# Kernel optimization log

Hardware: AMD Instinct MI355X
Metric: run time of the kernel (lower is better)

Reference implementation:

```python
import jax, jax.numpy as jnp
import numpy as np

TAU = 0.4
EPS = 1e-8


def setup_inputs() -> dict:
    key = jax.random.key(0)
    k1, k2 = jax.random.split(key)
    B, N, C, M = 4, 4096, 256, 2048
    l_feat = jax.random.normal(k1, (B, N, C), dtype=jnp.float32)
    g_feat = jax.random.normal(k2, (B, C, M), dtype=jnp.float32)
    return {"l_feat": l_feat, "g_feat": g_feat}


def reference(l_feat, g_feat):
    # l_feat: [B, N, C], g_feat: [B, C, M]
    # cosine similarity over channel dim C (torch CosineSimilarity, dim=2)
    l_norm = jnp.linalg.norm(l_feat, axis=2)          # [B, N]
    g_norm = jnp.linalg.norm(g_feat, axis=1)          # [B, M]
    dot = jnp.einsum('bnc,bcm->bnm', l_feat, g_feat)  # [B, N, M]
    cos_sim = dot / jnp.maximum(l_norm[:, :, None] * g_norm[:, None, :], EPS)
    sim = jnp.exp(cos_sim / TAU)                      # [B, N, M]
    # diag_embed(rowsum) followed by linalg.inv and bmm is exactly
    # row-wise division by the degree (row sum)
    sim = sim / jnp.sum(sim, axis=2, keepdims=True)
    # bmm(sim, g_feat^T): [B,N,M] x [B,M,C] -> [B,N,C]
    g_enh = jnp.einsum('bnm,bcm->bnc', sim, g_feat)
    return l_feat + g_enh
```

## Files before the change

kernel.cpp:

```cpp
#include <hip/hip_runtime.h>

#define B_ 4
#define N_ 4096
#define C_ 256
#define M_ 2048

typedef __attribute__((ext_vector_type(8))) short short8;
typedef __attribute__((ext_vector_type(4))) float f32x4;

union U16x8 { uint4 u4; unsigned short us[8]; short8 s8; };

__device__ __forceinline__ float bf2f(unsigned short h) {
    unsigned int u = ((unsigned int)h) << 16;
    return __builtin_bit_cast(float, u);
}
__device__ __forceinline__ unsigned short f2bf(float f) {
    unsigned int u = __builtin_bit_cast(unsigned int, f);
    u += 0x7FFFu + ((u >> 16) & 1u);
    return (unsigned short)(u >> 16);
}

#define GLB_AS(p) ((const __attribute__((address_space(1))) unsigned int*)(p))
#define LDS_AS(p) ((__attribute__((address_space(3))) unsigned int*)(p))

__global__ __launch_bounds__(256) void k_norm(const float* __restrict__ g,
                                              float* __restrict__ invgn) {
    __shared__ float red[4][64];
    const int b = blockIdx.y, m0 = blockIdx.x * 64;
    const int tid = threadIdx.x;
    const int ml = tid & 63, cq = tid >> 6;
    const float* gb = g + (size_t)b * C_ * M_ + m0 + ml;
    float ss = 0.f;
#pragma unroll 8
    for (int i = 0; i < 64; ++i) {
        float v = gb[(size_t)(cq * 64 + i) * M_];
        ss += v * v;
    }
    red[cq][ml] = ss;
    __syncthreads();
    if (cq == 0) {
        float t = red[0][ml] + red[1][ml] + red[2][ml] + red[3][ml];
        invgn[b * M_ + m0 + ml] = 1.f / fmaxf(sqrtf(t), 1e-8f);
    }
}

__global__ __launch_bounds__(256) void k_cast(const float* __restrict__ g,
                                              const float* __restrict__ invgn,
                                              unsigned short* __restrict__ gcm,
                                              unsigned short* __restrict__ gmc) {
    __shared__ unsigned short T[64 * 66];
    __shared__ float sInv[64];
    const int b = blockIdx.z, c0 = blockIdx.y * 64, m0 = blockIdx.x * 64;
    const int tid = threadIdx.x;
    if (tid < 64) sInv[tid] = invgn[b * M_ + m0 + tid];
    __syncthreads();
    const float* gbase = g + ((size_t)b * C_ + c0) * M_ + m0;
    unsigned short* gcmb = gcm + ((size_t)b * C_ + c0) * M_ + m0;
#pragma unroll
    for (int j = 0; j < 4; ++j) {
        int id = tid + 256 * j;
        int ci = id >> 4, mq = (id & 15) * 4;
        float4 v = *(const float4*)(gbase + (size_t)ci * M_ + mq);
        uint2 pk;
        pk.x = (unsigned)f2bf(v.x) | ((unsigned)f2bf(v.y) << 16);
        pk.y = (unsigned)f2bf(v.z) | ((unsigned)f2bf(v.w) << 16);
        *(uint2*)(gcmb + (size_t)ci * M_ + mq) = pk;
        T[ci * 66 + mq + 0] = f2bf(v.x * sInv[mq + 0]);
        T[ci * 66 + mq + 1] = f2bf(v.y * sInv[mq + 1]);
        T[ci * 66 + mq + 2] = f2bf(v.z * sInv[mq + 2]);
        T[ci * 66 + mq + 3] = f2bf(v.w * sInv[mq + 3]);
    }
    __syncthreads();
    unsigned short* gmcb = gmc + ((size_t)b * M_ + m0) * C_ + c0;
#pragma unroll
    for (int j = 0; j < 2; ++j) {
        int id = tid + 256 * j;
        int mr = id >> 3, cc8 = (id & 7) * 8;
        U16x8 t;
#pragma unroll
        for (int k = 0; k < 8; ++k) t.us[k] = T[(cc8 + k) * 66 + mr];
        *(uint4*)(gmcb + (size_t)mr * C_ + cc8) = t.u4;
    }
}

__global__ __launch_bounds__(256, 2) void k_main(
    const float* __restrict__ l,
    const unsigned short* __restrict__ gcm,
    const unsigned short* __restrict__ gmc,
    float* __restrict__ out)
{
    __shared__ __align__(16) unsigned short sGmc[64 * 256];
    __shared__ __align__(16) unsigned short sGcm[256 * 64];
    __shared__ __align__(16) unsigned short sP[32 * 72];
    __shared__ float sDen[2][32];

    const int tid = threadIdx.x;
    const int w = tid >> 6;
    const int lane = tid & 63;
    const int l15 = lane & 15;
    const int quad = lane >> 4;
    const int b = blockIdx.y;
    const int row0 = blockIdx.x * 32;
    const int rh = (w & 1) * 16;
    const int kh = w >> 1;

    int goffA[8], goffB[8];
#pragma unroll
    for (int i = 0; i < 8; ++i) {
        int p = (w * 8 + i) * 64 + lane;
        int rA = p >> 5;
        goffA[i] = rA * 256 + (((p & 31) ^ (rA & 31)) << 3);
        int rB = p >> 3;
        goffB[i] = rB * 2048 + (((p & 7) ^ (rB & 7)) << 3);
    }

    const unsigned short* gmc_b = gmc + (size_t)b * M_ * C_;
    const unsigned short* gcm_b = gcm + (size_t)b * C_ * M_;

    auto dmaA = [&](int m0) {
#pragma unroll
        for (int i = 0; i < 8; ++i)
            __builtin_amdgcn_global_load_lds(GLB_AS(gmc_b + (size_t)m0 * 256 + goffA[i]),
                                             LDS_AS(&sGmc[(w * 8 + i) * 512]), 16, 0, 0);
    };
    auto dmaB = [&](int m0) {
#pragma unroll
        for (int i = 0; i < 8; ++i)
            __builtin_amdgcn_global_load_lds(GLB_AS(gcm_b + (size_t)m0 + goffB[i]),
                                             LDS_AS(&sGcm[(w * 8 + i) * 512]), 16, 0, 0);
    };

    dmaA(0);
    dmaB(0);

    const float* lrow = l + ((size_t)b * N_ + row0 + rh + l15) * C_;
    U16x8 qt[8];
    float ss = 0.f;
#pragma unroll
    for (int kk = 0; kk < 8; ++kk) {
        float4 x0 = *(const float4*)(lrow + kk * 32 + quad * 8);
        float4 x1 = *(const float4*)(lrow + kk * 32 + quad * 8 + 4);
        ss += x0.x*x0.x + x0.y*x0.y + x0.z*x0.z + x0.w*x0.w;
        ss += x1.x*x1.x + x1.y*x1.y + x1.z*x1.z + x1.w*x1.w;
        qt[kk].us[0] = f2bf(x0.x); qt[kk].us[1] = f2bf(x0.y);
        qt[kk].us[2] = f2bf(x0.z); qt[kk].us[3] = f2bf(x0.w);
        qt[kk].us[4] = f2bf(x1.x); qt[kk].us[5] = f2bf(x1.y);
        qt[kk].us[6] = f2bf(x1.z); qt[kk].us[7] = f2bf(x1.w);
    }
    ss += __shfl_xor(ss, 16);
    ss += __shfl_xor(ss, 32);
    const float invl = 1.0f / fmaxf(sqrtf(ss), 1e-8f);
    short8 qf[8];
#pragma unroll
    for (int kk = 0; kk < 8; ++kk) {
        U16x8 t;
#pragma unroll
        for (int j = 0; j < 8; ++j) t.us[j] = f2bf(bf2f(qt[kk].us[j]) * invl);
        qf[kk] = t.s8;
    }

    __syncthreads();

    f32x4 zero = {0.f, 0.f, 0.f, 0.f};
    f32x4 o[2][4];
#pragma unroll
    for (int i = 0; i < 2; ++i)
#pragma unroll
        for (int j = 0; j < 4; ++j) o[i][j] = zero;
    float dl[4] = {0.f, 0.f, 0.f, 0.f};

    for (int mt = 0; mt < 32; ++mt) {
        f32x4 sa[2];
        sa[0] = zero; sa[1] = zero;
#pragma unroll
        for (int kk = 0; kk < 8; ++kk) {
#pragma unroll
            for (int ct = 0; ct < 2; ++ct) {
                const int row = kh * 32 + ct * 16 + l15;
                const int j = ((kk * 4 + quad) ^ (row & 31)) << 3;
                short8 bb = *(const short8*)&sGmc[row * 256 + j];
                sa[ct] = __builtin_amdgcn_mfma_f32_16x16x32_bf16(qf[kk], bb, sa[ct], 0, 0, 0);
            }
        }
#pragma unroll
        for (int ct = 0; ct < 2; ++ct)
#pragma unroll
            for (int r = 0; r < 4; ++r) {
                float p = exp2f(sa[ct][r] * 3.6067376022224085f);
                dl[r] += p;
                sP[(rh + quad * 4 + r) * 72 + kh * 32 + ct * 16 + l15] = f2bf(p);
            }
        __syncthreads();
        if (mt < 31) dmaA((mt + 1) * 64);

#pragma unroll
        for (int k2 = 0; k2 < 2; ++k2) {
            const int off = k2 * 32 + quad * 8;
            short8 a[2];
#pragma unroll
            for (int rt = 0; rt < 2; ++rt)
                a[rt] = *(const short8*)&sP[(rt * 16 + l15) * 72 + off];
#pragma unroll
            for (int ct = 0; ct < 4; ++ct) {
                const int crow = w * 64 + ct * 16 + l15;
                const int j = ((k2 * 4 + quad) ^ (crow & 7)) << 3;
                short8 bb = *(const short8*)&sGcm[crow * 64 + j];
#pragma unroll
                for (int rt = 0; rt < 2; ++rt)
                    o[rt][ct] = __builtin_amdgcn_mfma_f32_16x16x32_bf16(a[rt], bb, o[rt][ct], 0, 0, 0);
            }
        }
        __syncthreads();
        if (mt < 31) dmaB((mt + 1) * 64);
    }

#pragma unroll
    for (int r = 0; r < 4; ++r) {
        float d = dl[r];
        d += __shfl_xor(d, 1);
        d += __shfl_xor(d, 2);
        d += __shfl_xor(d, 4);
        d += __shfl_xor(d, 8);
        if (l15 == 0) sDen[kh][rh + quad * 4 + r] = d;
    }
    __syncthreads();

    const float* lb = l + ((size_t)b * N_ + row0) * C_;
    float* ob = out + ((size_t)b * N_ + row0) * C_;
#pragma unroll
    for (int rt = 0; rt < 2; ++rt) {
#pragma unroll
        for (int r = 0; r < 4; ++r) {
            const int row = rt * 16 + quad * 4 + r;
            const float inv = 1.f / (sDen[0][row] + sDen[1][row]);
            const size_t rbase = (size_t)row * C_;
#pragma unroll
            for (int ct = 0; ct < 4; ++ct) {
                const int c = w * 64 + ct * 16 + l15;
                ob[rbase + c] = lb[rbase + c] + o[rt][ct][r] * inv;
            }
        }
    }
}

extern "C" void kernel_launch(void* const* d_in, const int* in_sizes, int n_in,
                              void* d_out, int out_size, void* d_ws, size_t ws_size,
                              hipStream_t stream) {
    (void)in_sizes; (void)n_in; (void)out_size; (void)ws_size;
    const float* l = (const float*)d_in[0];
    const float* g = (const float*)d_in[1];
    float* outp = (float*)d_out;

    char* ws = (char*)d_ws;
    unsigned short* gmc = (unsigned short*)ws;
    unsigned short* gcm = (unsigned short*)(ws + (size_t)B_ * M_ * C_ * 2);
    float* invgn = (float*)(ws + 2 * (size_t)B_ * M_ * C_ * 2);

    k_norm<<<dim3(M_ / 64, B_), 256, 0, stream>>>(g, invgn);
    k_cast<<<dim3(M_ / 64, C_ / 64, B_), 256, 0, stream>>>(g, invgn, gcm, gmc);
    k_main<<<dim3(N_ / 32, B_), 256, 0, stream>>>(l, gcm, gmc, outp);
}
```

Before: 142.4 us.

## Repartition waves and use 32x32x16 MFMA for the second GEMM

Each wave now holds query fragments for all 32 rows and computes 16 key columns, so each LDS B-fragment read for the first GEMM feeds two MFMAs. The second GEMM switches from 16x16x32 to 32x32x16 bf16 MFMA with f32x16 accumulators, which cuts the number of LDS fragment loads and MFMA instructions per tile. The P buffer row stride changes to 68 and is read with split 8-byte loads, and the row-sum denominators are now reduced across four waves. The cost is more registers for the query fragments and the larger accumulators, which may hurt occupancy at the 2-block launch bound.

```diff
diff --git a/kernel.cpp b/kernel.cpp
--- a/kernel.cpp
+++ b/kernel.cpp
@@ -6,9 +6,11 @@
 #define M_ 2048
 
 typedef __attribute__((ext_vector_type(8))) short short8;
+typedef __attribute__((ext_vector_type(4))) short s16x4;
 typedef __attribute__((ext_vector_type(4))) float f32x4;
-
-union U16x8 { uint4 u4; unsigned short us[8]; short8 s8; };
+typedef __attribute__((ext_vector_type(16))) float f32x16;
+
+union U16x8 { uint4 u4; unsigned short us[8]; short8 s8; s16x4 s4[2]; };
 
 __device__ __forceinline__ float bf2f(unsigned short h) {
     unsigned int u = ((unsigned int)h) << 16;
@@ -18,6 +20,11 @@
     unsigned int u = __builtin_bit_cast(unsigned int, f);
     u += 0x7FFFu + ((u >> 16) & 1u);
     return (unsigned short)(u >> 16);
+}
+__device__ __forceinline__ short8 lds8(const unsigned short* p) {
+    s16x4 lo = *(const s16x4*)p;
+    s16x4 hi = *(const s16x4*)(p + 4);
+    return __builtin_shufflevector(lo, hi, 0, 1, 2, 3, 4, 5, 6, 7);
 }
 
 #define GLB_AS(p) ((const __attribute__((address_space(1))) unsigned int*)(p))
@@ -91,18 +98,18 @@
 {
     __shared__ __align__(16) unsigned short sGmc[64 * 256];
     __shared__ __align__(16) unsigned short sGcm[256 * 64];
-    __shared__ __align__(16) unsigned short sP[32 * 72];
-    __shared__ float sDen[2][32];
+    __shared__ __align__(16) unsigned short sP[32 * 68];
+    __shared__ float sDen[4][32];
 
     const int tid = threadIdx.x;
     const int w = tid >> 6;
     const int lane = tid & 63;
     const int l15 = lane & 15;
     const int quad = lane >> 4;
+    const int l31 = lane & 31;
+    const int h = lane >> 5;
     const int b = blockIdx.y;
     const int row0 = blockIdx.x * 32;
-    const int rh = (w & 1) * 16;
-    const int kh = w >> 1;
 
     int goffA[8], goffB[8];
 #pragma unroll
@@ -133,81 +140,75 @@
     dmaA(0);
     dmaB(0);
 
-    const float* lrow = l + ((size_t)b * N_ + row0 + rh + l15) * C_;
-    U16x8 qt[8];
-    float ss = 0.f;
-#pragma unroll
-    for (int kk = 0; kk < 8; ++kk) {
-        float4 x0 = *(const float4*)(lrow + kk * 32 + quad * 8);
-        float4 x1 = *(const float4*)(lrow + kk * 32 + quad * 8 + 4);
-        ss += x0.x*x0.x + x0.y*x0.y + x0.z*x0.z + x0.w*x0.w;
-        ss += x1.x*x1.x + x1.y*x1.y + x1.z*x1.z + x1.w*x1.w;
-        qt[kk].us[0] = f2bf(x0.x); qt[kk].us[1] = f2bf(x0.y);
-        qt[kk].us[2] = f2bf(x0.z); qt[kk].us[3] = f2bf(x0.w);
-        qt[kk].us[4] = f2bf(x1.x); qt[kk].us[5] = f2bf(x1.y);
-        qt[kk].us[6] = f2bf(x1.z); qt[kk].us[7] = f2bf(x1.w);
-    }
-    ss += __shfl_xor(ss, 16);
-    ss += __shfl_xor(ss, 32);
-    const float invl = 1.0f / fmaxf(sqrtf(ss), 1e-8f);
-    short8 qf[8];
-#pragma unroll
-    for (int kk = 0; kk < 8; ++kk) {
-        U16x8 t;
-#pragma unroll
-        for (int j = 0; j < 8; ++j) t.us[j] = f2bf(bf2f(qt[kk].us[j]) * invl);
-        qf[kk] = t.s8;
+    short8 qf[2][8];
+#pragma unroll
+    for (int rt = 0; rt < 2; ++rt) {
+        const float* lrow = l + ((size_t)b * N_ + row0 + rt * 16 + l15) * C_;
+        U16x8 qt[8];
+        float ss = 0.f;
+#pragma unroll
+        for (int kk = 0; kk < 8; ++kk) {
+            float4 x0 = *(const float4*)(lrow + kk * 32 + quad * 8);
+            float4 x1 = *(const float4*)(lrow + kk * 32 + quad * 8 + 4);
+            ss += x0.x*x0.x + x0.y*x0.y + x0.z*x0.z + x0.w*x0.w;
+            ss += x1.x*x1.x + x1.y*x1.y + x1.z*x1.z + x1.w*x1.w;
+            qt[kk].us[0] = f2bf(x0.x); qt[kk].us[1] = f2bf(x0.y);
+            qt[kk].us[2] = f2bf(x0.z); qt[kk].us[3] = f2bf(x0.w);
+            qt[kk].us[4] = f2bf(x1.x); qt[kk].us[5] = f2bf(x1.y);
+            qt[kk].us[6] = f2bf(x1.z); qt[kk].us[7] = f2bf(x1.w);
+        }
+        ss += __shfl_xor(ss, 16);
+        ss += __shfl_xor(ss, 32);
+        const float invl = 1.0f / fmaxf(sqrtf(ss), 1e-8f);
+#pragma unroll
+        for (int kk = 0; kk < 8; ++kk) {
+            U16x8 t;
+#pragma unroll
+            for (int j = 0; j < 8; ++j) t.us[j] = f2bf(bf2f(qt[kk].us[j]) * invl);
+            qf[rt][kk] = t.s8;
+        }
     }
 
     __syncthreads();
 
     f32x4 zero = {0.f, 0.f, 0.f, 0.f};
-    f32x4 o[2][4];
-#pragma unroll
-    for (int i = 0; i < 2; ++i)
-#pragma unroll
-        for (int j = 0; j < 4; ++j) o[i][j] = zero;
-    float dl[4] = {0.f, 0.f, 0.f, 0.f};
+    f32x16 o[2];
+#pragma unroll
+    for (int i = 0; i < 16; ++i) { o[0][i] = 0.f; o[1][i] = 0.f; }
+    float dl[2][4] = {{0.f,0.f,0.f,0.f},{0.f,0.f,0.f,0.f}};
 
     for (int mt = 0; mt < 32; ++mt) {
         f32x4 sa[2];
         sa[0] = zero; sa[1] = zero;
+        const int g1row = w * 16 + l15;
 #pragma unroll
         for (int kk = 0; kk < 8; ++kk) {
-#pragma unroll
-            for (int ct = 0; ct < 2; ++ct) {
-                const int row = kh * 32 + ct * 16 + l15;
-                const int j = ((kk * 4 + quad) ^ (row & 31)) << 3;
-                short8 bb = *(const short8*)&sGmc[row * 256 + j];
-                sa[ct] = __builtin_amdgcn_mfma_f32_16x16x32_bf16(qf[kk], bb, sa[ct], 0, 0, 0);
-            }
-        }
-#pragma unroll
-        for (int ct = 0; ct < 2; ++ct)
+            const int j = ((kk * 4 + quad) ^ (g1row & 31)) << 3;
+            short8 bb = *(const short8*)&sGmc[g1row * 256 + j];
+            sa[0] = __builtin_amdgcn_mfma_f32_16x16x32_bf16(qf[0][kk], bb, sa[0], 0, 0, 0);
+            sa[1] = __builtin_amdgcn_mfma_f32_16x16x32_bf16(qf[1][kk], bb, sa[1], 0, 0, 0);
+        }
+#pragma unroll
+        for (int rt = 0; rt < 2; ++rt)
 #pragma unroll
             for (int r = 0; r < 4; ++r) {
-                float p = exp2f(sa[ct][r] * 3.6067376022224085f);
-                dl[r] += p;
-                sP[(rh + quad * 4 + r) * 72 + kh * 32 + ct * 16 + l15] = f2bf(p);
+                float p = exp2f(sa[rt][r] * 3.6067376022224085f);
+                dl[rt][r] += p;
+                sP[(rt * 16 + quad * 4 + r) * 68 + w * 16 + l15] = f2bf(p);
             }
         __syncthreads();
+
         if (mt < 31) dmaA((mt + 1) * 64);
 
 #pragma unroll
-        for (int k2 = 0; k2 < 2; ++k2) {
-            const int off = k2 * 32 + quad * 8;
-            short8 a[2];
-#pragma unroll
-            for (int rt = 0; rt < 2; ++rt)
-                a[rt] = *(const short8*)&sP[(rt * 16 + l15) * 72 + off];
-#pragma unroll
-            for (int ct = 0; ct < 4; ++ct) {
-                const int crow = w * 64 + ct * 16 + l15;
-                const int j = ((k2 * 4 + quad) ^ (crow & 7)) << 3;
-                short8 bb = *(const short8*)&sGcm[crow * 64 + j];
-#pragma unroll
-                for (int rt = 0; rt < 2; ++rt)
-                    o[rt][ct] = __builtin_amdgcn_mfma_f32_16x16x32_bf16(a[rt], bb, o[rt][ct], 0, 0, 0);
+        for (int kk = 0; kk < 4; ++kk) {
+            short8 a = lds8(&sP[l31 * 68 + kk * 16 + h * 8]);
+#pragma unroll
+            for (int ct = 0; ct < 2; ++ct) {
+                const int c = w * 64 + ct * 32 + l31;
+                const int j = ((kk * 2 + h) ^ (c & 7)) << 3;
+                short8 bb = *(const short8*)&sGcm[c * 64 + j];
+                o[ct] = __builtin_amdgcn_mfma_f32_32x32x16_bf16(a, bb, o[ct], 0, 0, 0);
             }
         }
         __syncthreads();
@@ -215,30 +216,29 @@
     }
 
 #pragma unroll
-    for (int r = 0; r < 4; ++r) {
-        float d = dl[r];
-        d += __shfl_xor(d, 1);
-        d += __shfl_xor(d, 2);
-        d += __shfl_xor(d, 4);
-        d += __shfl_xor(d, 8);
-        if (l15 == 0) sDen[kh][rh + quad * 4 + r] = d;
-    }
+    for (int rt = 0; rt < 2; ++rt)
+#pragma unroll
+        for (int r = 0; r < 4; ++r) {
+            float d = dl[rt][r];
+            d += __shfl_xor(d, 1);
+            d += __shfl_xor(d, 2);
+            d += __shfl_xor(d, 4);
+            d += __shfl_xor(d, 8);
+            if (l15 == 0) sDen[w][rt * 16 + quad * 4 + r] = d;
+        }
     __syncthreads();
 
     const float* lb = l + ((size_t)b * N_ + row0) * C_;
     float* ob = out + ((size_t)b * N_ + row0) * C_;
 #pragma unroll
-    for (int rt = 0; rt < 2; ++rt) {
-#pragma unroll
-        for (int r = 0; r < 4; ++r) {
-            const int row = rt * 16 + quad * 4 + r;
-            const float inv = 1.f / (sDen[0][row] + sDen[1][row]);
-            const size_t rbase = (size_t)row * C_;
-#pragma unroll
-            for (int ct = 0; ct < 4; ++ct) {
-                const int c = w * 64 + ct * 16 + l15;
-                ob[rbase + c] = lb[rbase + c] + o[rt][ct][r] * inv;
-            }
+    for (int reg = 0; reg < 16; ++reg) {
+        const int row = (reg & 3) + 8 * (reg >> 2) + 4 * h;
+        const float inv = 1.f / (sDen[0][row] + sDen[1][row] + sDen[2][row] + sDen[3][row]);
+        const size_t rbase = (size_t)row * C_;
+#pragma unroll
+        for (int ct = 0; ct < 2; ++ct) {
+            const int c = w * 64 + ct * 32 + l31;
+            ob[rbase + c] = lb[rbase + c] + o[ct][reg] * inv;
         }
     }
 }
```

New measurement: 147.3 us. +3.4%, slower.
